# Optimization experiments

Measured on AMD Instinct MI355X. Metric: run time of the kernel, lower is better.

Reference implementation:

```python
import jax, jax.numpy as jnp
import numpy as np

B, N, D = 2, 2048, 256
H = 8
HD = D // H
SCALE = HD ** 0.5  # NOTE: source MULTIPLIES by sqrt(head_dim)
EPS = 1e-5
DFF = 4 * D


def setup_inputs() -> dict:
    key = jax.random.key(0)
    ks = jax.random.split(key, 9)
    s = lambda fan_in: 1.0 / np.sqrt(fan_in)
    return {
        "x": jax.random.normal(ks[0], (B, N, D), dtype=jnp.float32),
        # weights stored [in, out] (transposed torch Linear)
        "qkv_w": jax.random.normal(ks[1], (D, 3 * D), dtype=jnp.float32) * s(D),
        "proj_w": jax.random.normal(ks[2], (D, D), dtype=jnp.float32) * s(D),
        "proj_b": jax.random.normal(ks[3], (D,), dtype=jnp.float32) * 0.01,
        "fc1_w": jax.random.normal(ks[4], (D, DFF), dtype=jnp.float32) * s(D),
        "fc1_b": jax.random.normal(ks[5], (DFF,), dtype=jnp.float32) * 0.01,
        "fc2_w": jax.random.normal(ks[6], (DFF, D), dtype=jnp.float32) * s(DFF),
        "fc2_b": jax.random.normal(ks[7], (D,), dtype=jnp.float32) * 0.01,
        "ln1_g": jnp.ones((D,), dtype=jnp.float32),
        "ln1_b": jnp.zeros((D,), dtype=jnp.float32),
    }


def _layernorm(x, g, b):
    mu = jnp.mean(x, axis=-1, keepdims=True)
    var = jnp.mean(jnp.square(x - mu), axis=-1, keepdims=True)
    return (x - mu) * jax.lax.rsqrt(var + EPS) * g + b


def reference(x, qkv_w, proj_w, proj_b, fc1_w, fc1_b, fc2_w, fc2_b, ln1_g, ln1_b):
    b, n, d = x.shape
    # --- MHA ---
    qkv = (x @ qkv_w).reshape(b, n, 3, H, HD)
    q = qkv[:, :, 0].transpose(0, 2, 1, 3)  # [B,H,N,HD]
    k = qkv[:, :, 1].transpose(0, 2, 1, 3)
    v = qkv[:, :, 2].transpose(0, 2, 1, 3)
    att = jnp.einsum("bhqd,bhkd->bhqk", q, k) * SCALE  # multiplied, per source
    att = jax.nn.softmax(att, axis=-1)
    out = jnp.einsum("bhqk,bhkd->bhqd", att, v)
    out = out.transpose(0, 2, 1, 3).reshape(b, n, d)
    out = out @ proj_w + proj_b
    # --- post-norm residual ---
    net = _layernorm(out + x, ln1_g, ln1_b)
    shortcut = net
    # --- MLP (NO activation in source forward) ---
    net = (net @ fc1_w + fc1_b) @ fc2_w + fc2_b
    return net + shortcut
```

## Files before the change

kernel.cpp:

```cpp
#include <hip/hip_runtime.h>


typedef __attribute__((ext_vector_type(8))) short short8;
typedef __attribute__((ext_vector_type(8))) _Float16 half8;
typedef __attribute__((ext_vector_type(4))) short bf16x4;
typedef __attribute__((ext_vector_type(4))) float floatx4;
typedef __attribute__((ext_vector_type(2))) unsigned int uint2v;
typedef unsigned short u16;

#define MFMA32(a,b,c)  __builtin_amdgcn_mfma_f32_16x16x32_bf16((a),(b),(c),0,0,0)
#define MFMAF16(a,b,c) __builtin_amdgcn_mfma_f32_16x16x32_f16((a),(b),(c),0,0,0)
#if __has_builtin(__builtin_amdgcn_mfma_f32_16x16x16_bf16)
#define MFMAPV(a,b,c) __builtin_amdgcn_mfma_f32_16x16x16_bf16((a),(b),(c),0,0,0)
#else
#define MFMAPV(a,b,c) __builtin_amdgcn_mfma_f32_16x16x16bf16_1k((a),(b),(c),0,0,0)
#endif
#define CLF 8.1615404f

#if __has_builtin(__builtin_amdgcn_exp2f)
#define EX2(x) __builtin_amdgcn_exp2f(x)
#else
#define EX2(x) exp2f(x)
#endif

__device__ __forceinline__ float bf2f(u16 u) { return __uint_as_float(((unsigned)u) << 16); }
__device__ __forceinline__ u16 f2bf(float f) {
  unsigned u = __float_as_uint(f);
  u += 0x7fffu + ((u >> 16) & 1u);
  return (u16)(u >> 16);
}
__device__ __forceinline__ u16 f2h(float f) {
  _Float16 h = (_Float16)f;
  return *(u16*)&h;
}
__device__ __forceinline__ unsigned pkbf2(float a, float b) {
#if __has_builtin(__builtin_amdgcn_perm)
  return __builtin_amdgcn_perm(__float_as_uint(b) + 0x8000u,
                               __float_as_uint(a) + 0x8000u, 0x07060302u);
#else
  return (unsigned)f2bf(a) | ((unsigned)f2bf(b) << 16);
#endif
}
__device__ __forceinline__ void gll16(const void* g, void* l) {
  __builtin_amdgcn_global_load_lds((const __attribute__((address_space(1))) void*)g,
                                   (__attribute__((address_space(3))) void*)l, 16, 0, 0);
}

__global__ __launch_bounds__(256) void prep_k(
    const void* __restrict__ x, const void* __restrict__ qkv_w,
    const void* __restrict__ proj_w, const void* __restrict__ fc1_w,
    const void* __restrict__ fc2_w, const void* __restrict__ proj_b,
    const void* __restrict__ fc1_b, const void* __restrict__ fc2_b,
    const void* __restrict__ ln_g, const void* __restrict__ ln_b,
    u16* __restrict__ x_hi, u16* __restrict__ x_lo,
    u16* __restrict__ wq_hi, u16* __restrict__ wq_lo,
    u16* __restrict__ wt_proj, u16* __restrict__ wt_fc1, u16* __restrict__ wt_fc2,
    u16* __restrict__ b_proj, u16* __restrict__ b_fc1, u16* __restrict__ b_fc2,
    u16* __restrict__ g_ln, u16* __restrict__ bb_ln)
{
  const int lane = threadIdx.x & 63;
  const float probe = bf2f(((const u16*)qkv_w)[lane]);
  const bool f32 = __ballot(!(fabsf(probe) < 1000.0f)) != 0ull;
  const int bid = blockIdx.x, tid = threadIdx.x;
  #define RD(p, i) (f32 ? ((const float*)(p))[i] : bf2f(((const u16*)(p))[i]))
  if (bid < 4096) {
    const size_t i = (size_t)bid * 256 + tid;
    const float f = RD(x, i); const u16 h = f2bf(f);
    x_hi[i] = h; x_lo[i] = f2bf(f - bf2f(h));
  } else if (bid < 4864) {
    const int idx = (bid - 4096) * 256 + tid;
    const int n = idx >> 8, k = idx & 255;
    const float f = RD(qkv_w, (size_t)k * 768 + n); const u16 h = f2bf(f);
    wq_hi[idx] = h; wq_lo[idx] = f2bf(f - bf2f(h));
  } else if (bid < 5120) {
    const int idx = (bid - 4864) * 256 + tid;
    wt_proj[idx] = f2bf(RD(proj_w, (size_t)(idx & 255) * 256 + (idx >> 8)));
  } else if (bid < 6144) {
    const int idx = (bid - 5120) * 256 + tid;
    wt_fc1[idx] = f2bf(RD(fc1_w, (size_t)(idx & 255) * 1024 + (idx >> 8)));
  } else if (bid < 7168) {
    const int idx = (bid - 6144) * 256 + tid;
    wt_fc2[idx] = f2bf(RD(fc2_w, (size_t)(idx & 1023) * 256 + (idx >> 10)));
  } else {
    const int j = (bid - 7168) * 256 + tid;
    if (j < 256)       b_proj[j]        = f2bf(RD(proj_b, j));
    else if (j < 1280) b_fc1[j - 256]   = f2bf(RD(fc1_b, j - 256));
    else if (j < 1536) b_fc2[j - 1280]  = f2bf(RD(fc2_b, j - 1280));
    else if (j < 1792) g_ln[j - 1536]   = f2bf(RD(ln_g, j - 1536));
    else               bb_ln[j - 1792]  = f2bf(RD(ln_b, j - 1792));
  }
  #undef RD
}

template<int TW, int EPI, bool BIAS, bool RES, bool SPLIT, bool COMB>
__global__ __launch_bounds__(256) void gemm_k(
    const u16* __restrict__ A, const u16* __restrict__ Bt,
    const u16* __restrict__ A2, const u16* __restrict__ B2,
    const u16* __restrict__ bias, const u16* __restrict__ res,
    void* __restrict__ out0, u16* __restrict__ aux1, u16* __restrict__ aux3,
    const float* __restrict__ muc,
    int M, int Nn, int K)
{
  constexpr int BT = TW * 32;
  constexpr int NC = TW / 2;
  __shared__ __align__(16) short As[BT][40];
  __shared__ __align__(16) short Bs[BT][40];
  __shared__ __align__(16) short As2[SPLIT ? BT : 1][40];
  __shared__ __align__(16) short Bs2[SPLIT ? BT : 1][40];
  __shared__ __align__(16) u16 Vt[(EPI == 2) ? 64 * 72 : 1];
  const int tid = threadIdx.x;
  const int m0 = blockIdx.y * BT, n0 = blockIdx.x * BT;
  const bool sp = SPLIT && (n0 < 512);
  const int wid = tid >> 6, lane = tid & 63;
  const int wm = (wid >> 1) * (TW * 16), wn = (wid & 1) * (TW * 16);
  const int lm = lane & 15, quad = lane >> 4;

  floatx4 zero = {0.f, 0.f, 0.f, 0.f};
  floatx4 acc[TW][TW];
#pragma unroll
  for (int i = 0; i < TW; ++i)
#pragma unroll
    for (int j = 0; j < TW; ++j) acc[i][j] = zero;

  auto comb8 = [&](int t, int col8) -> short8 {
    const size_t o = (size_t)t * 256 + col8;
    const int h = col8 >> 5;
    const float m0_ = muc[t * 8 + h],          m1_ = muc[32768 + t * 8 + h];
    const float m2_ = muc[65536 + t * 8 + h],  m3_ = muc[98304 + t * 8 + h];
    const float M = fmaxf(fmaxf(m0_, m1_), fmaxf(m2_, m3_));
    float w0 = EX2(m0_ - M), w1 = EX2(m1_ - M), w2 = EX2(m2_ - M), w3 = EX2(m3_ - M);
    const float inv = 1.f / (w0 + w1 + w2 + w3);
    w0 *= inv; w1 *= inv; w2 *= inv; w3 *= inv;
    short8 a0 = *(const short8*)&A[o],  a1 = *(const short8*)&A[o + 1048576];
    short8 a2 = *(const short8*)&A2[o], a3 = *(const short8*)&A2[o + 1048576];
    float v[8];
#pragma unroll
    for (int j = 0; j < 8; ++j)
      v[j] = w0 * bf2f(a0[j]) + w1 * bf2f(a1[j]) + w2 * bf2f(a2[j]) + w3 * bf2f(a3[j]);
    uint2v uu0 = {pkbf2(v[0], v[1]), pkbf2(v[2], v[3])};
    uint2v uu1 = {pkbf2(v[4], v[5]), pkbf2(v[6], v[7])};
    short8 r;
    *(uint2v*)&r = uu0; *((uint2v*)&r + 1) = uu1;
    return r;
  };

  int srow[NC], soff[NC];
#pragma unroll
  for (int c = 0; c < NC; ++c) {
    const int cid = tid * NC + c;
    srow[c] = cid >> 2; soff[c] = (cid & 3) * 8;
  }
  short8 ra[NC], rb[NC], ra2[NC], rb2[NC];
#pragma unroll
  for (int c = 0; c < NC; ++c) {
    const size_t gb = (size_t)(n0 + srow[c]) * K + soff[c];
    rb[c] = *(const short8*)&Bt[gb];
    if (COMB) ra[c] = comb8(m0 + srow[c], soff[c]);
    else      ra[c] = *(const short8*)&A[(size_t)(m0 + srow[c]) * K + soff[c]];
    if (sp) {
      ra2[c] = *(const short8*)&A2[(size_t)(m0 + srow[c]) * K + soff[c]];
      rb2[c] = *(const short8*)&B2[gb];
    }
  }
  for (int k0 = 0; k0 < K; k0 += 32) {
    if (k0) __syncthreads();
#pragma unroll
    for (int c = 0; c < NC; ++c) {
      *(short8*)&As[srow[c]][soff[c]] = ra[c];
      *(short8*)&Bs[srow[c]][soff[c]] = rb[c];
      if (sp) {
        *(short8*)&As2[srow[c]][soff[c]] = ra2[c];
        *(short8*)&Bs2[srow[c]][soff[c]] = rb2[c];
      }
    }
    __syncthreads();
    if (k0 + 32 < K) {
#pragma unroll
      for (int c = 0; c < NC; ++c) {
        const size_t gb = (size_t)(n0 + srow[c]) * K + k0 + 32 + soff[c];
        rb[c] = *(const short8*)&Bt[gb];
        if (COMB) ra[c] = comb8(m0 + srow[c], k0 + 32 + soff[c]);
        else      ra[c] = *(const short8*)&A[(size_t)(m0 + srow[c]) * K + k0 + 32 + soff[c]];
        if (sp) {
          ra2[c] = *(const short8*)&A2[(size_t)(m0 + srow[c]) * K + k0 + 32 + soff[c]];
          rb2[c] = *(const short8*)&B2[gb];
        }
      }
    }
    short8 fa[TW], fb[TW], fa2[TW], fb2[TW];
#pragma unroll
    for (int t = 0; t < TW; ++t) {
      fa[t] = *(const short8*)&As[wm + t * 16 + lm][quad * 8];
      fb[t] = *(const short8*)&Bs[wn + t * 16 + lm][quad * 8];
      if (sp) {
        fa2[t] = *(const short8*)&As2[wm + t * 16 + lm][quad * 8];
        fb2[t] = *(const short8*)&Bs2[wn + t * 16 + lm][quad * 8];
      }
    }
#pragma unroll
    for (int i = 0; i < TW; ++i)
#pragma unroll
      for (int j = 0; j < TW; ++j) {
        if (sp) {
          acc[i][j] = MFMA32(fa[i], fb2[j], acc[i][j]);
          acc[i][j] = MFMA32(fa2[i], fb[j], acc[i][j]);
        }
        acc[i][j] = MFMA32(fa[i], fb[j], acc[i][j]);
      }
  }

  if (EPI == 2 && n0 >= 512) {
    __syncthreads();
#pragma unroll
    for (int i = 0; i < TW; ++i)
#pragma unroll
      for (int j = 0; j < TW; ++j)
#pragma unroll
        for (int r = 0; r < 4; ++r)
          Vt[(wn + j * 16 + lm) * 72 + wm + i * 16 + quad * 4 + r] = f2bf(acc[i][j][r]);
    __syncthreads();
    const int bb = m0 >> 11, n = m0 & 2047;
#pragma unroll
    for (int pass = 0; pass < 2; ++pass) {
      const int dl = (tid >> 3) + pass * 32;
      const int oct = tid & 7;
      const int col = n0 - 512 + dl;
      const int d = col & 31, hh = col >> 5;
      short8 v = *(const short8*)&Vt[dl * 72 + oct * 8];
      *(short8*)&((u16*)out0)[(size_t)((bb * 8 + hh) * 32 + d) * 2048 + n + oct * 8] = v;
    }
    return;
  }

#pragma unroll
  for (int i = 0; i < TW; ++i) {
    const int rowb = m0 + wm + i * 16 + quad * 4;
#pragma unroll
    for (int j = 0; j < TW; ++j) {
      const int col = n0 + wn + j * 16 + lm;
      const float bv = BIAS ? bf2f(bias[col]) : 0.f;
#pragma unroll
      for (int r = 0; r < 4; ++r) {
        const int row = rowb + r;
        float v = acc[i][j][r] + bv;
        const size_t o = (size_t)row * Nn + col;
        if (RES) v += bf2f(res[o]);
        if (EPI == 0) {
          ((float*)out0)[o] = v;
        } else if (EPI == 1) {
          ((u16*)out0)[o] = f2bf(v);
        } else {
          if (col < 256) aux1[(size_t)row * 256 + col] = f2h(v);
          else           aux3[(size_t)row * 256 + (col - 256)] = f2h(v);
        }
      }
    }
  }
}

template<int CHUNKS>
__global__ __launch_bounds__(256) void attn_k(
    const u16* __restrict__ qf16, const u16* __restrict__ kf16,
    const u16* __restrict__ vt, u16* __restrict__ outp, u16* __restrict__ out23,
    float* __restrict__ mu)
{
  __shared__ __align__(16) u16 Ks[2][64][32];
  __shared__ __align__(16) u16 Vs[2][32][64];
  const int tid = threadIdx.x, wid = tid >> 6, lane = tid & 63;
  const int lm = lane & 15, quad = lane >> 4;
  const int bid = blockIdx.x;
  const int chunk = (CHUNKS > 1) ? (bid >> 9) : 0;
  const int qblk = bid & 31, bh = (bid >> 5) & 15;
  const int b = bh >> 3, h = bh & 7;
  const int q0 = qblk * 64 + wid * 16;
  const size_t tb = (size_t)b * 2048;
  const int NT = 32 / CHUNKS;
  const int kofs = chunk * (2048 / CHUNKS);

  half8 qh;
  { size_t off = (tb + q0 + lm) * 256 + h * 32 + quad * 8;
    qh = *(const half8*)&qf16[off]; }

  const int kkey = tid >> 2, kg = tid & 3;
  const size_t kb = (tb + kofs + kkey) * 256 + h * 32 + kg * 8;
  const int vd = tid >> 3, vp = tid & 7, vk8 = vp ^ (vd & 7);
  const size_t vb = (size_t)(bh * 32 + vd) * 2048 + kofs + vk8 * 8;

  gll16(kf16 + kb, (u16*)Ks + tid * 8);
  gll16(vt  + vb,  (u16*)Vs + tid * 8);

  float mrun = -1e30f, lrun = 0.f;
  floatx4 o0 = {0.f,0.f,0.f,0.f}, o1 = {0.f,0.f,0.f,0.f};

  for (int kt = 0; kt < NT; ++kt) {
    const int buf = kt & 1;
    __syncthreads();
    if (kt < NT - 1) {
      const int nb = (buf ^ 1) * 2048;
      const size_t ko = (size_t)(kt + 1) * 16384;
      const size_t vo = (size_t)(kt + 1) * 64;
      gll16(kf16 + kb + ko, (u16*)Ks + nb + tid * 8);
      gll16(vt  + vb + vo,  (u16*)Vs + nb + tid * 8);
    }

    floatx4 z[4];
#pragma unroll
    for (int kf = 0; kf < 4; ++kf) {
      half8 khf = *(const half8*)&Ks[buf][kf * 16 + lm][quad * 8];
      floatx4 zz = {0.f,0.f,0.f,0.f};
      z[kf] = MFMAF16(khf, qh, zz);
    }
    float zm = fmaxf(fmaxf(fmaxf(z[0][0], z[0][1]), fmaxf(z[0][2], z[0][3])),
               fmaxf(fmaxf(z[1][0], z[1][1]), fmaxf(z[1][2], z[1][3])));
    zm = fmaxf(zm, fmaxf(fmaxf(fmaxf(z[2][0], z[2][1]), fmaxf(z[2][2], z[2][3])),
                   fmaxf(fmaxf(z[3][0], z[3][1]), fmaxf(z[3][2], z[3][3]))));
    zm = fmaxf(zm, __shfl_xor(zm, 16));
    zm = fmaxf(zm, __shfl_xor(zm, 32));
    const float mn = fmaxf(mrun, zm);
    const float alpha = EX2((mrun - mn) * CLF);
    const float mc = mn * CLF;
    mrun = mn;
    float ls = 0.f;
    bf16x4 pb[4];
#pragma unroll
    for (int kf = 0; kf < 4; ++kf) {
      const float p0 = EX2(__builtin_fmaf(z[kf][0], CLF, -mc));
      const float p1 = EX2(__builtin_fmaf(z[kf][1], CLF, -mc));
      const float p2 = EX2(__builtin_fmaf(z[kf][2], CLF, -mc));
      const float p3 = EX2(__builtin_fmaf(z[kf][3], CLF, -mc));
      ls += (p0 + p1) + (p2 + p3);
      uint2v uu = {pkbf2(p0, p1), pkbf2(p2, p3)};
      pb[kf] = *(bf16x4*)&uu;
    }
    ls += __shfl_xor(ls, 16);
    ls += __shfl_xor(ls, 32);
    lrun = lrun * alpha + ls;
#pragma unroll
    for (int r = 0; r < 4; ++r) { o0[r] *= alpha; o1[r] *= alpha; }
    const u16* vbase = (const u16*)Vs + buf * 2048;
#pragma unroll
    for (int kf = 0; kf < 4; ++kf) {
      const int k8 = 2 * kf + (quad >> 1);
      const int d0 = lm, d1 = 16 + lm;
      bf16x4 vf0 = *(const bf16x4*)(vbase + (d0 * 8 + (k8 ^ (d0 & 7))) * 8 + (quad & 1) * 4);
      bf16x4 vf1 = *(const bf16x4*)(vbase + (d1 * 8 + (k8 ^ (d1 & 7))) * 8 + (quad & 1) * 4);
      o0 = MFMAPV(vf0, pb[kf], o0);
      o1 = MFMAPV(vf1, pb[kf], o1);
    }
  }
  const float inv = 1.0f / lrun;
  const size_t tok = tb + q0 + lm;
  u16* dst = ((CHUNKS > 2 && chunk >= 2) ? out23 : outp) + (size_t)(chunk & 1) * 1048576;
  const size_t rowo = tok * 256 + h * 32;
#pragma unroll
  for (int r = 0; r < 4; ++r) {
    dst[rowo + quad * 4 + r]      = f2bf(o0[r] * inv);
    dst[rowo + 16 + quad * 4 + r] = f2bf(o1[r] * inv);
  }
  if (CHUNKS > 1 && quad == 0)
    mu[chunk * 32768 + tok * 8 + h] = __builtin_fmaf(mrun, CLF, __log2f(lrun));
}

template<int CHUNKS>
__global__ __launch_bounds__(256) void combine_k(u16* __restrict__ d,
                                                 const u16* __restrict__ e,
                                                 const float* __restrict__ mu)
{
  const int t = blockIdx.x, c = threadIdx.x, h = c >> 5;
  const size_t o = (size_t)t * 256 + c;
  float m[CHUNKS];
  float M = -1e30f;
#pragma unroll
  for (int i = 0; i < CHUNKS; ++i) { m[i] = mu[i * 32768 + t * 8 + h]; M = fmaxf(M, m[i]); }
  float wsum = 0.f, acc = 0.f;
#pragma unroll
  for (int i = 0; i < CHUNKS; ++i) {
    const float w = EX2(m[i] - M);
    const u16 v = (i < 2) ? d[o + (size_t)i * 1048576] : e[o + (size_t)(i - 2) * 1048576];
    wsum += w; acc += w * bf2f(v);
  }
  d[o] = f2bf(acc / wsum);
}

__global__ __launch_bounds__(256) void ln_k(const float* __restrict__ pf,
                                            const u16* __restrict__ xh,
                                            const u16* __restrict__ xl,
                                            const u16* __restrict__ g,
                                            const u16* __restrict__ bta,
                                            u16* __restrict__ net)
{
  const int t = blockIdx.x, c = threadIdx.x;
  const size_t o = (size_t)t * 256 + c;
  float v = pf[o] + bf2f(xh[o]) + bf2f(xl[o]);
  float s = v, s2 = v * v;
#pragma unroll
  for (int d = 1; d < 64; d <<= 1) { s += __shfl_xor(s, d); s2 += __shfl_xor(s2, d); }
  __shared__ float ss[4], ss2[4];
  const int w = c >> 6;
  if ((c & 63) == 0) { ss[w] = s; ss2[w] = s2; }
  __syncthreads();
  s = ss[0] + ss[1] + ss[2] + ss[3];
  s2 = ss2[0] + ss2[1] + ss2[2] + ss2[3];
  const float mu = s * (1.f / 256.f);
  const float var = s2 * (1.f / 256.f) - mu * mu;
  const float is = rsqrtf(var + 1e-5f);
  net[o] = f2bf((v - mu) * is * bf2f(g[c]) + bf2f(bta[c]));
}

extern "C" void kernel_launch(void* const* d_in, const int* in_sizes, int n_in,
                              void* d_out, int out_size, void* d_ws, size_t ws_size,
                              hipStream_t stream) {
  const void* x      = d_in[0];
  const void* qkv_w  = d_in[1];
  const void* proj_w = d_in[2];
  const void* proj_b = d_in[3];
  const void* fc1_w  = d_in[4];
  const void* fc1_b  = d_in[5];
  const void* fc2_w  = d_in[6];
  const void* fc2_b  = d_in[7];
  const void* ln_g   = d_in[8];
  const void* ln_b   = d_in[9];

  char* ws = (char*)d_ws;
  u16* b_proj  = (u16*)(ws + 4096);
  u16* b_fc1   = (u16*)(ws + 8192);
  u16* b_fc2   = (u16*)(ws + 12288);
  u16* g_ln    = (u16*)(ws + 16384);
  u16* bb_ln   = (u16*)(ws + 20480);
  u16* wq_hi   = (u16*)(ws + 131072);
  u16* wq_lo   = (u16*)(ws + 524288);
  u16* wt_proj = (u16*)(ws + 917504);
  u16* wt_fc1  = (u16*)(ws + 1048576);
  u16* wt_fc2  = (u16*)(ws + 1572864);
  u16* x_hi    = (u16*)(ws + 2097152);
  u16* x_lo    = (u16*)(ws + 4194304);
  u16* q_f16   = (u16*)(ws + 6291456);
  u16* k_f16   = (u16*)(ws + 10485760);
  u16* vt      = (u16*)(ws + 14680064);
  float* mu    = (float*)(ws + 16777216);
  u16* out23   = (u16*)(ws + 17301504);
  u16* attn    = (u16*)d_out;
  float* projf = (float*)(ws + 6291456);
  u16* net     = (u16*)(ws + 14680064);
  u16* hbuf    = (u16*)(ws + 2097152);

  const bool sk4 = ws_size >= (17301504 + 4194304);
  const bool sk2 = ws_size >= (16777216 + 262144);

  prep_k<<<7176, 256, 0, stream>>>(x, qkv_w, proj_w, fc1_w, fc2_w,
                                   proj_b, fc1_b, fc2_b, ln_g, ln_b,
                                   x_hi, x_lo, wq_hi, wq_lo, wt_proj, wt_fc1, wt_fc2,
                                   b_proj, b_fc1, b_fc2, g_ln, bb_ln);

  gemm_k<2, 2, false, false, true, false><<<dim3(12, 64), 256, 0, stream>>>(
      x_hi, wq_hi, x_lo, wq_lo, nullptr, nullptr, vt, q_f16, k_f16,
      nullptr, 4096, 768, 256);
  if (sk4) {
    attn_k<4><<<2048, 256, 0, stream>>>(q_f16, k_f16, vt, attn, out23, mu);
    gemm_k<2, 0, true, false, false, true><<<dim3(4, 64), 256, 0, stream>>>(
        attn, wt_proj, out23, nullptr, b_proj, nullptr, projf,
        nullptr, nullptr, mu, 4096, 256, 256);
  } else if (sk2) {
    attn_k<2><<<1024, 256, 0, stream>>>(q_f16, k_f16, vt, attn, nullptr, mu);
    combine_k<2><<<4096, 256, 0, stream>>>(attn, nullptr, mu);
    gemm_k<2, 0, true, false, false, false><<<dim3(4, 64), 256, 0, stream>>>(
        attn, wt_proj, nullptr, nullptr, b_proj, nullptr, projf,
        nullptr, nullptr, nullptr, 4096, 256, 256);
  } else {
    attn_k<1><<<512, 256, 0, stream>>>(q_f16, k_f16, vt, attn, nullptr, nullptr);
    gemm_k<2, 0, true, false, false, false><<<dim3(4, 64), 256, 0, stream>>>(
        attn, wt_proj, nullptr, nullptr, b_proj, nullptr, projf,
        nullptr, nullptr, nullptr, 4096, 256, 256);
  }
  ln_k<<<4096, 256, 0, stream>>>(projf, x_hi, x_lo, g_ln, bb_ln, net);
  gemm_k<2, 1, true, false, false, false><<<dim3(16, 64), 256, 0, stream>>>(
      net, wt_fc1, nullptr, nullptr, b_fc1, nullptr, hbuf,
      nullptr, nullptr, nullptr, 4096, 1024, 256);
  gemm_k<2, 0, true, true, false, false><<<dim3(4, 64), 256, 0, stream>>>(
      hbuf, wt_fc2, nullptr, nullptr, b_fc2, net, d_out,
      nullptr, nullptr, nullptr, 4096, 256, 1024);
}
```

Before: 155.3 us.

## Switch pipeline from split bf16 hi/lo to single fp16 operands

```diff
diff --git a/kernel.cpp b/kernel.cpp
--- a/kernel.cpp
+++ b/kernel.cpp
@@ -3,17 +3,17 @@
 
 typedef __attribute__((ext_vector_type(8))) short short8;
 typedef __attribute__((ext_vector_type(8))) _Float16 half8;
-typedef __attribute__((ext_vector_type(4))) short bf16x4;
+typedef __attribute__((ext_vector_type(4))) _Float16 half4;
+typedef __attribute__((ext_vector_type(2))) __fp16 fp16x2;
 typedef __attribute__((ext_vector_type(4))) float floatx4;
 typedef __attribute__((ext_vector_type(2))) unsigned int uint2v;
 typedef unsigned short u16;
 
-#define MFMA32(a,b,c)  __builtin_amdgcn_mfma_f32_16x16x32_bf16((a),(b),(c),0,0,0)
-#define MFMAF16(a,b,c) __builtin_amdgcn_mfma_f32_16x16x32_f16((a),(b),(c),0,0,0)
-#if __has_builtin(__builtin_amdgcn_mfma_f32_16x16x16_bf16)
-#define MFMAPV(a,b,c) __builtin_amdgcn_mfma_f32_16x16x16_bf16((a),(b),(c),0,0,0)
+#define MFMAG(a,b,c)  __builtin_amdgcn_mfma_f32_16x16x32_f16((a),(b),(c),0,0,0)
+#if __has_builtin(__builtin_amdgcn_mfma_f32_16x16x16_f16)
+#define MFMAPV(a,b,c) __builtin_amdgcn_mfma_f32_16x16x16_f16((a),(b),(c),0,0,0)
 #else
-#define MFMAPV(a,b,c) __builtin_amdgcn_mfma_f32_16x16x16bf16_1k((a),(b),(c),0,0,0)
+#define MFMAPV(a,b,c) __builtin_amdgcn_mfma_f32_16x16x16f16((a),(b),(c),0,0,0)
 #endif
 #define CLF 8.1615404f
 
@@ -24,21 +24,14 @@
 #endif
 
 __device__ __forceinline__ float bf2f(u16 u) { return __uint_as_float(((unsigned)u) << 16); }
-__device__ __forceinline__ u16 f2bf(float f) {
-  unsigned u = __float_as_uint(f);
-  u += 0x7fffu + ((u >> 16) & 1u);
-  return (u16)(u >> 16);
-}
-__device__ __forceinline__ u16 f2h(float f) {
-  _Float16 h = (_Float16)f;
-  return *(u16*)&h;
-}
-__device__ __forceinline__ unsigned pkbf2(float a, float b) {
-#if __has_builtin(__builtin_amdgcn_perm)
-  return __builtin_amdgcn_perm(__float_as_uint(b) + 0x8000u,
-                               __float_as_uint(a) + 0x8000u, 0x07060302u);
+__device__ __forceinline__ float h2f(u16 u) { _Float16 h = *(_Float16*)&u; return (float)h; }
+__device__ __forceinline__ u16 f2h(float f) { _Float16 h = (_Float16)f; return *(u16*)&h; }
+__device__ __forceinline__ unsigned pkh2(float a, float b) {
+#if __has_builtin(__builtin_amdgcn_cvt_pkrtz)
+  fp16x2 h = __builtin_amdgcn_cvt_pkrtz(a, b);
+  return *(unsigned*)&h;
 #else
-  return (unsigned)f2bf(a) | ((unsigned)f2bf(b) << 16);
+  return (unsigned)f2h(a) | ((unsigned)f2h(b) << 16);
 #endif
 }
 __device__ __forceinline__ void gll16(const void* g, void* l) {
@@ -52,8 +45,7 @@
     const void* __restrict__ fc2_w, const void* __restrict__ proj_b,
     const void* __restrict__ fc1_b, const void* __restrict__ fc2_b,
     const void* __restrict__ ln_g, const void* __restrict__ ln_b,
-    u16* __restrict__ x_hi, u16* __restrict__ x_lo,
-    u16* __restrict__ wq_hi, u16* __restrict__ wq_lo,
+    u16* __restrict__ x_f, u16* __restrict__ wq_f,
     u16* __restrict__ wt_proj, u16* __restrict__ wt_fc1, u16* __restrict__ wt_fc2,
     u16* __restrict__ b_proj, u16* __restrict__ b_fc1, u16* __restrict__ b_fc2,
     u16* __restrict__ g_ln, u16* __restrict__ bb_ln)
@@ -65,37 +57,34 @@
   #define RD(p, i) (f32 ? ((const float*)(p))[i] : bf2f(((const u16*)(p))[i]))
   if (bid < 4096) {
     const size_t i = (size_t)bid * 256 + tid;
-    const float f = RD(x, i); const u16 h = f2bf(f);
-    x_hi[i] = h; x_lo[i] = f2bf(f - bf2f(h));
+    x_f[i] = f2h(RD(x, i));
   } else if (bid < 4864) {
     const int idx = (bid - 4096) * 256 + tid;
     const int n = idx >> 8, k = idx & 255;
-    const float f = RD(qkv_w, (size_t)k * 768 + n); const u16 h = f2bf(f);
-    wq_hi[idx] = h; wq_lo[idx] = f2bf(f - bf2f(h));
+    wq_f[idx] = f2h(RD(qkv_w, (size_t)k * 768 + n));
   } else if (bid < 5120) {
     const int idx = (bid - 4864) * 256 + tid;
-    wt_proj[idx] = f2bf(RD(proj_w, (size_t)(idx & 255) * 256 + (idx >> 8)));
+    wt_proj[idx] = f2h(RD(proj_w, (size_t)(idx & 255) * 256 + (idx >> 8)));
   } else if (bid < 6144) {
     const int idx = (bid - 5120) * 256 + tid;
-    wt_fc1[idx] = f2bf(RD(fc1_w, (size_t)(idx & 255) * 1024 + (idx >> 8)));
+    wt_fc1[idx] = f2h(RD(fc1_w, (size_t)(idx & 255) * 1024 + (idx >> 8)));
   } else if (bid < 7168) {
     const int idx = (bid - 6144) * 256 + tid;
-    wt_fc2[idx] = f2bf(RD(fc2_w, (size_t)(idx & 1023) * 256 + (idx >> 10)));
+    wt_fc2[idx] = f2h(RD(fc2_w, (size_t)(idx & 1023) * 256 + (idx >> 10)));
   } else {
     const int j = (bid - 7168) * 256 + tid;
-    if (j < 256)       b_proj[j]        = f2bf(RD(proj_b, j));
-    else if (j < 1280) b_fc1[j - 256]   = f2bf(RD(fc1_b, j - 256));
-    else if (j < 1536) b_fc2[j - 1280]  = f2bf(RD(fc2_b, j - 1280));
-    else if (j < 1792) g_ln[j - 1536]   = f2bf(RD(ln_g, j - 1536));
-    else               bb_ln[j - 1792]  = f2bf(RD(ln_b, j - 1792));
+    if (j < 256)       b_proj[j]        = f2h(RD(proj_b, j));
+    else if (j < 1280) b_fc1[j - 256]   = f2h(RD(fc1_b, j - 256));
+    else if (j < 1536) b_fc2[j - 1280]  = f2h(RD(fc2_b, j - 1280));
+    else if (j < 1792) g_ln[j - 1536]   = f2h(RD(ln_g, j - 1536));
+    else               bb_ln[j - 1792]  = f2h(RD(ln_b, j - 1792));
   }
   #undef RD
 }
 
-template<int TW, int EPI, bool BIAS, bool RES, bool SPLIT, bool COMB>
+template<int TW, int EPI, bool BIAS, bool RES, bool COMB>
 __global__ __launch_bounds__(256) void gemm_k(
-    const u16* __restrict__ A, const u16* __restrict__ Bt,
-    const u16* __restrict__ A2, const u16* __restrict__ B2,
+    const u16* __restrict__ A, const u16* __restrict__ Bt, const u16* __restrict__ A2,
     const u16* __restrict__ bias, const u16* __restrict__ res,
     void* __restrict__ out0, u16* __restrict__ aux1, u16* __restrict__ aux3,
     const float* __restrict__ muc,
@@ -103,14 +92,11 @@
 {
   constexpr int BT = TW * 32;
   constexpr int NC = TW / 2;
-  __shared__ __align__(16) short As[BT][40];
-  __shared__ __align__(16) short Bs[BT][40];
-  __shared__ __align__(16) short As2[SPLIT ? BT : 1][40];
-  __shared__ __align__(16) short Bs2[SPLIT ? BT : 1][40];
+  __shared__ __align__(16) u16 As[BT][40];
+  __shared__ __align__(16) u16 Bs[BT][40];
   __shared__ __align__(16) u16 Vt[(EPI == 2) ? 64 * 72 : 1];
   const int tid = threadIdx.x;
   const int m0 = blockIdx.y * BT, n0 = blockIdx.x * BT;
-  const bool sp = SPLIT && (n0 < 512);
   const int wid = tid >> 6, lane = tid & 63;
   const int wm = (wid >> 1) * (TW * 16), wn = (wid & 1) * (TW * 16);
   const int lm = lane & 15, quad = lane >> 4;
@@ -136,9 +122,10 @@
     float v[8];
 #pragma unroll
     for (int j = 0; j < 8; ++j)
-      v[j] = w0 * bf2f(a0[j]) + w1 * bf2f(a1[j]) + w2 * bf2f(a2[j]) + w3 * bf2f(a3[j]);
-    uint2v uu0 = {pkbf2(v[0], v[1]), pkbf2(v[2], v[3])};
-    uint2v uu1 = {pkbf2(v[4], v[5]), pkbf2(v[6], v[7])};
+      v[j] = w0 * h2f((u16)a0[j]) + w1 * h2f((u16)a1[j])
+           + w2 * h2f((u16)a2[j]) + w3 * h2f((u16)a3[j]);
+    uint2v uu0 = {pkh2(v[0], v[1]), pkh2(v[2], v[3])};
+    uint2v uu1 = {pkh2(v[4], v[5]), pkh2(v[6], v[7])};
     short8 r;
     *(uint2v*)&r = uu0; *((uint2v*)&r + 1) = uu1;
     return r;
@@ -150,17 +137,12 @@
     const int cid = tid * NC + c;
     srow[c] = cid >> 2; soff[c] = (cid & 3) * 8;
   }
-  short8 ra[NC], rb[NC], ra2[NC], rb2[NC];
+  short8 ra[NC], rb[NC];
 #pragma unroll
   for (int c = 0; c < NC; ++c) {
-    const size_t gb = (size_t)(n0 + srow[c]) * K + soff[c];
-    rb[c] = *(const short8*)&Bt[gb];
+    rb[c] = *(const short8*)&Bt[(size_t)(n0 + srow[c]) * K + soff[c]];
     if (COMB) ra[c] = comb8(m0 + srow[c], soff[c]);
     else      ra[c] = *(const short8*)&A[(size_t)(m0 + srow[c]) * K + soff[c]];
-    if (sp) {
-      ra2[c] = *(const short8*)&A2[(size_t)(m0 + srow[c]) * K + soff[c]];
-      rb2[c] = *(const short8*)&B2[gb];
-    }
   }
   for (int k0 = 0; k0 < K; k0 += 32) {
     if (k0) __syncthreads();
@@ -168,45 +150,27 @@
     for (int c = 0; c < NC; ++c) {
       *(short8*)&As[srow[c]][soff[c]] = ra[c];
       *(short8*)&Bs[srow[c]][soff[c]] = rb[c];
-      if (sp) {
-        *(short8*)&As2[srow[c]][soff[c]] = ra2[c];
-        *(short8*)&Bs2[srow[c]][soff[c]] = rb2[c];
-      }
     }
     __syncthreads();
     if (k0 + 32 < K) {
 #pragma unroll
       for (int c = 0; c < NC; ++c) {
-        const size_t gb = (size_t)(n0 + srow[c]) * K + k0 + 32 + soff[c];
-        rb[c] = *(const short8*)&Bt[gb];
+        rb[c] = *(const short8*)&Bt[(size_t)(n0 + srow[c]) * K + k0 + 32 + soff[c]];
         if (COMB) ra[c] = comb8(m0 + srow[c], k0 + 32 + soff[c]);
         else      ra[c] = *(const short8*)&A[(size_t)(m0 + srow[c]) * K + k0 + 32 + soff[c]];
-        if (sp) {
-          ra2[c] = *(const short8*)&A2[(size_t)(m0 + srow[c]) * K + k0 + 32 + soff[c]];
-          rb2[c] = *(const short8*)&B2[gb];
-        }
       }
     }
-    short8 fa[TW], fb[TW], fa2[TW], fb2[TW];
+    half8 fa[TW], fb[TW];
 #pragma unroll
     for (int t = 0; t < TW; ++t) {
-      fa[t] = *(const short8*)&As[wm + t * 16 + lm][quad * 8];
-      fb[t] = *(const short8*)&Bs[wn + t * 16 + lm][quad * 8];
-      if (sp) {
-        fa2[t] = *(const short8*)&As2[wm + t * 16 + lm][quad * 8];
-        fb2[t] = *(const short8*)&Bs2[wn + t * 16 + lm][quad * 8];
-      }
+      fa[t] = *(const half8*)&As[wm + t * 16 + lm][quad * 8];
+      fb[t] = *(const half8*)&Bs[wn + t * 16 + lm][quad * 8];
     }
 #pragma unroll
     for (int i = 0; i < TW; ++i)
 #pragma unroll
-      for (int j = 0; j < TW; ++j) {
-        if (sp) {
-          acc[i][j] = MFMA32(fa[i], fb2[j], acc[i][j]);
-          acc[i][j] = MFMA32(fa2[i], fb[j], acc[i][j]);
-        }
-        acc[i][j] = MFMA32(fa[i], fb[j], acc[i][j]);
-      }
+      for (int j = 0; j < TW; ++j)
+        acc[i][j] = MFMAG(fa[i], fb[j], acc[i][j]);
   }
 
   if (EPI == 2 && n0 >= 512) {
@@ -217,7 +181,7 @@
       for (int j = 0; j < TW; ++j)
 #pragma unroll
         for (int r = 0; r < 4; ++r)
-          Vt[(wn + j * 16 + lm) * 72 + wm + i * 16 + quad * 4 + r] = f2bf(acc[i][j][r]);
+          Vt[(wn + j * 16 + lm) * 72 + wm + i * 16 + quad * 4 + r] = f2h(acc[i][j][r]);
     __syncthreads();
     const int bb = m0 >> 11, n = m0 & 2047;
 #pragma unroll
@@ -238,17 +202,17 @@
 #pragma unroll
     for (int j = 0; j < TW; ++j) {
       const int col = n0 + wn + j * 16 + lm;
-      const float bv = BIAS ? bf2f(bias[col]) : 0.f;
+      const float bv = BIAS ? h2f(bias[col]) : 0.f;
 #pragma unroll
       for (int r = 0; r < 4; ++r) {
         const int row = rowb + r;
         float v = acc[i][j][r] + bv;
         const size_t o = (size_t)row * Nn + col;
-        if (RES) v += bf2f(res[o]);
+        if (RES) v += h2f(res[o]);
         if (EPI == 0) {
           ((float*)out0)[o] = v;
         } else if (EPI == 1) {
-          ((u16*)out0)[o] = f2bf(v);
+          ((u16*)out0)[o] = f2h(v);
         } else {
           if (col < 256) aux1[(size_t)row * 256 + col] = f2h(v);
           else           aux3[(size_t)row * 256 + (col - 256)] = f2h(v);
@@ -308,7 +272,7 @@
     for (int kf = 0; kf < 4; ++kf) {
       half8 khf = *(const half8*)&Ks[buf][kf * 16 + lm][quad * 8];
       floatx4 zz = {0.f,0.f,0.f,0.f};
-      z[kf] = MFMAF16(khf, qh, zz);
+      z[kf] = MFMAG(khf, qh, zz);
     }
     float zm = fmaxf(fmaxf(fmaxf(z[0][0], z[0][1]), fmaxf(z[0][2], z[0][3])),
                fmaxf(fmaxf(z[1][0], z[1][1]), fmaxf(z[1][2], z[1][3])));
@@ -321,7 +285,7 @@
     const float mc = mn * CLF;
     mrun = mn;
     float ls = 0.f;
-    bf16x4 pb[4];
+    half4 pb[4];
 #pragma unroll
     for (int kf = 0; kf < 4; ++kf) {
       const float p0 = EX2(__builtin_fmaf(z[kf][0], CLF, -mc));
@@ -329,8 +293,8 @@
       const float p2 = EX2(__builtin_fmaf(z[kf][2], CLF, -mc));
       const float p3 = EX2(__builtin_fmaf(z[kf][3], CLF, -mc));
       ls += (p0 + p1) + (p2 + p3);
-      uint2v uu = {pkbf2(p0, p1), pkbf2(p2, p3)};
-      pb[kf] = *(bf16x4*)&uu;
+      uint2v uu = {pkh2(p0, p1), pkh2(p2, p3)};
+      pb[kf] = *(half4*)&uu;
     }
     ls += __shfl_xor(ls, 16);
     ls += __shfl_xor(ls, 32);
@@ -342,8 +306,8 @@
     for (int kf = 0; kf < 4; ++kf) {
       const int k8 = 2 * kf + (quad >> 1);
       const int d0 = lm, d1 = 16 + lm;
-      bf16x4 vf0 = *(const bf16x4*)(vbase + (d0 * 8 + (k8 ^ (d0 & 7))) * 8 + (quad & 1) * 4);
-      bf16x4 vf1 = *(const bf16x4*)(vbase + (d1 * 8 + (k8 ^ (d1 & 7))) * 8 + (quad & 1) * 4);
+      half4 vf0 = *(const half4*)(vbase + (d0 * 8 + (k8 ^ (d0 & 7))) * 8 + (quad & 1) * 4);
+      half4 vf1 = *(const half4*)(vbase + (d1 * 8 + (k8 ^ (d1 & 7))) * 8 + (quad & 1) * 4);
       o0 = MFMAPV(vf0, pb[kf], o0);
       o1 = MFMAPV(vf1, pb[kf], o1);
     }
@@ -354,8 +318,8 @@
   const size_t rowo = tok * 256 + h * 32;
 #pragma unroll
   for (int r = 0; r < 4; ++r) {
-    dst[rowo + quad * 4 + r]      = f2bf(o0[r] * inv);
-    dst[rowo + 16 + quad * 4 + r] = f2bf(o1[r] * inv);
+    dst[rowo + quad * 4 + r]      = f2h(o0[r] * inv);
+    dst[rowo + 16 + quad * 4 + r] = f2h(o1[r] * inv);
   }
   if (CHUNKS > 1 && quad == 0)
     mu[chunk * 32768 + tok * 8 + h] = __builtin_fmaf(mrun, CLF, __log2f(lrun));
@@ -377,21 +341,20 @@
   for (int i = 0; i < CHUNKS; ++i) {
     const float w = EX2(m[i] - M);
     const u16 v = (i < 2) ? d[o + (size_t)i * 1048576] : e[o + (size_t)(i - 2) * 1048576];
-    wsum += w; acc += w * bf2f(v);
-  }
-  d[o] = f2bf(acc / wsum);
+    wsum += w; acc += w * h2f(v);
+  }
+  d[o] = f2h(acc / wsum);
 }
 
 __global__ __launch_bounds__(256) void ln_k(const float* __restrict__ pf,
                                             const u16* __restrict__ xh,
-                                            const u16* __restrict__ xl,
                                             const u16* __restrict__ g,
                                             const u16* __restrict__ bta,
                                             u16* __restrict__ net)
 {
   const int t = blockIdx.x, c = threadIdx.x;
   const size_t o = (size_t)t * 256 + c;
-  float v = pf[o] + bf2f(xh[o]) + bf2f(xl[o]);
+  float v = pf[o] + h2f(xh[o]);
   float s = v, s2 = v * v;
 #pragma unroll
   for (int d = 1; d < 64; d <<= 1) { s += __shfl_xor(s, d); s2 += __shfl_xor(s2, d); }
@@ -404,7 +367,7 @@
   const float mu = s * (1.f / 256.f);
   const float var = s2 * (1.f / 256.f) - mu * mu;
   const float is = rsqrtf(var + 1e-5f);
-  net[o] = f2bf((v - mu) * is * bf2f(g[c]) + bf2f(bta[c]));
+  net[o] = f2h((v - mu) * is * h2f(g[c]) + h2f(bta[c]));
 }
 
 extern "C" void kernel_launch(void* const* d_in, const int* in_sizes, int n_in,
@@ -427,56 +390,52 @@
   u16* b_fc2   = (u16*)(ws + 12288);
   u16* g_ln    = (u16*)(ws + 16384);
   u16* bb_ln   = (u16*)(ws + 20480);
-  u16* wq_hi   = (u16*)(ws + 131072);
-  u16* wq_lo   = (u16*)(ws + 524288);
-  u16* wt_proj = (u16*)(ws + 917504);
-  u16* wt_fc1  = (u16*)(ws + 1048576);
-  u16* wt_fc2  = (u16*)(ws + 1572864);
-  u16* x_hi    = (u16*)(ws + 2097152);
-  u16* x_lo    = (u16*)(ws + 4194304);
-  u16* q_f16   = (u16*)(ws + 6291456);
-  u16* k_f16   = (u16*)(ws + 10485760);
-  u16* vt      = (u16*)(ws + 14680064);
-  float* mu    = (float*)(ws + 16777216);
-  u16* out23   = (u16*)(ws + 17301504);
+  u16* wq_f    = (u16*)(ws + 131072);
+  u16* wt_proj = (u16*)(ws + 524288);
+  u16* wt_fc1  = (u16*)(ws + 655360);
+  u16* wt_fc2  = (u16*)(ws + 1179648);
+  u16* x_f     = (u16*)(ws + 2097152);
+  u16* q_f16   = (u16*)(ws + 4194304);
+  u16* k_f16   = (u16*)(ws + 6291456);
+  u16* vt      = (u16*)(ws + 8388608);
+  float* mu    = (float*)(ws + 10485760);
+  u16* out23   = (u16*)(ws + 11010048);
   u16* attn    = (u16*)d_out;
-  float* projf = (float*)(ws + 6291456);
-  u16* net     = (u16*)(ws + 14680064);
+  float* projf = (float*)(ws + 4194304);
+  u16* net     = (u16*)(ws + 11010048);
   u16* hbuf    = (u16*)(ws + 2097152);
 
-  const bool sk4 = ws_size >= (17301504 + 4194304);
-  const bool sk2 = ws_size >= (16777216 + 262144);
+  const bool sk4 = ws_size >= 15204352;
+  const bool sk2 = ws_size >= 11010048;
 
   prep_k<<<7176, 256, 0, stream>>>(x, qkv_w, proj_w, fc1_w, fc2_w,
                                    proj_b, fc1_b, fc2_b, ln_g, ln_b,
-                                   x_hi, x_lo, wq_hi, wq_lo, wt_proj, wt_fc1, wt_fc2,
+                                   x_f, wq_f, wt_proj, wt_fc1, wt_fc2,
                                    b_proj, b_fc1, b_fc2, g_ln, bb_ln);
 
-  gemm_k<2, 2, false, false, true, false><<<dim3(12, 64), 256, 0, stream>>>(
-      x_hi, wq_hi, x_lo, wq_lo, nullptr, nullptr, vt, q_f16, k_f16,
-      nullptr, 4096, 768, 256);
+  gemm_k<2, 2, false, false, false><<<dim3(12, 64), 256, 0, stream>>>(
+      x_f, wq_f, nullptr, nullptr, nullptr, vt, q_f16, k_f16, nullptr, 4096, 768, 256);
   if (sk4) {
     attn_k<4><<<2048, 256, 0, stream>>>(q_f16, k_f16, vt, attn, out23, mu);
-    gemm_k<2, 0, true, false, false, true><<<dim3(4, 64), 256, 0, stream>>>(
-        attn, wt_proj, out23, nullptr, b_proj, nullptr, projf,
-        nullptr, nullptr, mu, 4096, 256, 256);
+    gemm_k<2, 0, true, false, true><<<dim3(4, 64), 256, 0, stream>>>(
+        attn, wt_proj, out23, b_proj, nullptr, projf, nullptr, nullptr, mu, 4096, 256, 256);
   } else if (sk2) {
     attn_k<2><<<1024, 256, 0, stream>>>(q_f16, k_f16, vt, attn, nullptr, mu);
     combine_k<2><<<4096, 256, 0, stream>>>(attn, nullptr, mu);
-    gemm_k<2, 0, true, false, false, false><<<dim3(4, 64), 256, 0, stream>>>(
-        attn, wt_proj, nullptr, nullptr, b_proj, nullptr, projf,
-        nullptr, nullptr, nullptr, 4096, 256, 256);
+    gemm_k<2, 0, true, false, false><<<dim3(4, 64), 256, 0, stream>>>(
+        attn, wt_proj, nullptr, b_proj, nullptr, projf, nullptr, nullptr, nullptr,
+        4096, 256, 256);
   } else {
     attn_k<1><<<512, 256, 0, stream>>>(q_f16, k_f16, vt, attn, nullptr, nullptr);
-    gemm_k<2, 0, true, false, false, false><<<dim3(4, 64), 256, 0, stream>>>(
-        attn, wt_proj, nullptr, nullptr, b_proj, nullptr, projf,
-        nullptr, nullptr, nullptr, 4096, 256, 256);
-  }
-  ln_k<<<4096, 256, 0, stream>>>(projf, x_hi, x_lo, g_ln, bb_ln, net);
-  gemm_k<2, 1, true, false, false, false><<<dim3(16, 64), 256, 0, stream>>>(
-      net, wt_fc1, nullptr, nullptr, b_fc1, nullptr, hbuf,
-      nullptr, nullptr, nullptr, 4096, 1024, 256);
-  gemm_k<2, 0, true, true, false, false><<<dim3(4, 64), 256, 0, stream>>>(
-      hbuf, wt_fc2, nullptr, nullptr, b_fc2, net, d_out,
-      nullptr, nullptr, nullptr, 4096, 256, 1024);
-}
+    gemm_k<2, 0, true, false, false><<<dim3(4, 64), 256, 0, stream>>>(
+        attn, wt_proj, nullptr, b_proj, nullptr, projf, nullptr, nullptr, nullptr,
+        4096, 256, 256);
+  }
+  ln_k<<<4096, 256, 0, stream>>>(projf, x_f, g_ln, bb_ln, net);
+  gemm_k<2, 1, true, false, false><<<dim3(16, 64), 256, 0, stream>>>(
+      net, wt_fc1, nullptr, b_fc1, nullptr, hbuf, nullptr, nullptr, nullptr,
+      4096, 1024, 256);
+  gemm_k<2, 0, true, true, false><<<dim3(4, 64), 256, 0, stream>>>(
+      hbuf, wt_fc2, nullptr, b_fc2, net, d_out, nullptr, nullptr, nullptr,
+      4096, 256, 1024);
+}
```

After: 148.9 us. -4.1%, faster.
